# Performance work log

Hardware: AMD Instinct MI355X
Metric: run time of the kernel (lower is better)

## Reference

```python
import jax, jax.numpy as jnp
import numpy as np

N = 100000   # nodes
E = 1600000  # edges (avg degree 16)
D = 128      # feature dim (in_dim = out_dim = 128)


def setup_inputs() -> dict:
    key = jax.random.key(0)
    k0, k1, k2, k3, k4, k5 = jax.random.split(key, 6)
    x = jax.random.normal(k0, (N, D), dtype=jnp.float32)
    edge_index = jax.random.randint(k1, (2, E), 0, N, dtype=jnp.int32)
    # GCNConv linear weights (PyG stores lin.weight [out,in]; math is x @ W.T, here W:[in,out])
    s1 = 1.0 / np.sqrt(D)
    W1 = jax.random.uniform(k2, (D, D), jnp.float32, -s1, s1)
    b1 = jnp.zeros((D,), jnp.float32)
    W2 = jax.random.uniform(k3, (D, D), jnp.float32, -s1, s1)
    b2 = jnp.zeros((D,), jnp.float32)
    return {"x": x, "edge_index": edge_index, "W1": W1, "b1": b1, "W2": W2, "b2": b2}


def reference(x, edge_index, W1, b1, W2, b2):
    n = x.shape[0]
    idt = edge_index.dtype
    loop = jnp.arange(n, dtype=idt)
    src = jnp.concatenate([edge_index[0], loop])  # message sources
    dst = jnp.concatenate([edge_index[1], loop])  # aggregation targets
    # improved=True -> self-loop fill value 2.0; edge_weight=None -> ones
    w = jnp.concatenate([jnp.ones((edge_index.shape[1],), x.dtype),
                         jnp.full((n,), 2.0, x.dtype)])
    deg = jax.ops.segment_sum(w, dst, num_segments=n)
    dinv = jnp.where(deg > 0, jax.lax.rsqrt(deg), 0.0)
    norm = dinv[src] * w * dinv[dst]  # [E+N] symmetric GCN normalization

    def conv(h, W, b):
        h = h @ W  # [N, D] dense transform
        agg = jax.ops.segment_sum(norm[:, None] * h[src], dst, num_segments=n)
        return agg + b

    h = conv(x, W1, b1)        # conv1
    for _ in range(4):
        h = conv(h, W2, b2)
    return h
```

## Files before the change

### kernel.cpp

```cpp
#include <hip/hip_runtime.h>
#include <hip/hip_fp16.h>

#define D 128

typedef _Float16 half8 __attribute__((ext_vector_type(8)));
typedef float floatx4 __attribute__((ext_vector_type(4)));


__device__ inline void acc_h4(float& ax, float& ay, float& az, float& aw,
                              float w, uint2 raw) {
    __half2 h01 = *reinterpret_cast<const __half2*>(&raw.x);
    __half2 h23 = *reinterpret_cast<const __half2*>(&raw.y);
    ax = fmaf(w, __low2float(h01), ax);
    ay = fmaf(w, __high2float(h01), ay);
    az = fmaf(w, __low2float(h23), az);
    aw = fmaf(w, __high2float(h23), aw);
}


__global__ void k_zero(int* __restrict__ p, int n) {
    int i = blockIdx.x * 256 + threadIdx.x;
    if (i < n) p[i] = 0;
}

__global__ void k_count(const int* __restrict__ dst, int* __restrict__ cnt,
                        int* __restrict__ rank, int e) {
    int i = blockIdx.x * 256 + threadIdx.x;
    if (i < e) rank[i] = atomicAdd(&cnt[dst[i]], 1);
}

__global__ void k_f2h(const float* __restrict__ in, __half* __restrict__ out, int n8) {
    int i = blockIdx.x * 256 + threadIdx.x;
    if (i < n8) {
        const float4* p = (const float4*)in + (size_t)i * 2;
        float4 a = p[0], b = p[1];
        __half2 h0 = __float22half2_rn(make_float2(a.x, a.y));
        __half2 h1 = __float22half2_rn(make_float2(a.z, a.w));
        __half2 h2 = __float22half2_rn(make_float2(b.x, b.y));
        __half2 h3 = __float22half2_rn(make_float2(b.z, b.w));
        uint4 o;
        o.x = *(unsigned*)&h0; o.y = *(unsigned*)&h1;
        o.z = *(unsigned*)&h2; o.w = *(unsigned*)&h3;
        ((uint4*)out)[i] = o;
    }
}


__global__ __launch_bounds__(256) void k_scanA(const int* __restrict__ cnt,
                                               int* __restrict__ partials,
                                               float* __restrict__ dinv, int n) {
    __shared__ int s[256];
    int b = blockIdx.x, t = threadIdx.x;
    int i0 = b * 512 + t * 2;
    int v = 0;
    if (i0 < n) {
        int c0 = cnt[i0];
        v += c0;
        dinv[i0] = 1.0f / sqrtf((float)(c0 + 2));
    }
    if (i0 + 1 < n) {
        int c1 = cnt[i0 + 1];
        v += c1;
        dinv[i0 + 1] = 1.0f / sqrtf((float)(c1 + 2));
    }
    s[t] = v;
    __syncthreads();
    for (int off = 128; off > 0; off >>= 1) {
        if (t < off) s[t] += s[t + off];
        __syncthreads();
    }
    if (t == 0) partials[b] = s[0];
}

__global__ __launch_bounds__(512) void k_scanB(const int* __restrict__ partials,
                                               int* __restrict__ base,
                                               int* __restrict__ off_n, int nb) {
    __shared__ int s[512];
    int t = threadIdx.x;
    int v = (t < nb) ? partials[t] : 0;
    s[t] = v;
    __syncthreads();
    for (int off = 1; off < 512; off <<= 1) {
        int x = (t >= off) ? s[t - off] : 0;
        __syncthreads();
        s[t] += x;
        __syncthreads();
    }
    if (t < nb) base[t] = s[t] - v;
    if (t == nb - 1) off_n[0] = s[t];
}

__global__ __launch_bounds__(256) void k_scanC(const int* __restrict__ cnt,
                                               const int* __restrict__ base,
                                               int* __restrict__ offsets, int n) {
    __shared__ int s[256];
    int b = blockIdx.x, t = threadIdx.x;
    int i0 = b * 512 + t * 2;
    int v0 = (i0 < n) ? cnt[i0] : 0;
    int v1 = (i0 + 1 < n) ? cnt[i0 + 1] : 0;
    int sum = v0 + v1;
    s[t] = sum;
    __syncthreads();
    for (int off = 1; off < 256; off <<= 1) {
        int x = (t >= off) ? s[t - off] : 0;
        __syncthreads();
        s[t] += x;
        __syncthreads();
    }
    int excl = s[t] - sum + base[b];
    if (i0 < n) offsets[i0] = excl;
    if (i0 + 1 < n) offsets[i0 + 1] = excl + v0;
}

__global__ void k_fill(const int* __restrict__ src, const int* __restrict__ dst,
                       const int* __restrict__ rank, const int* __restrict__ offsets,
                       const float* __restrict__ dinv, int2* __restrict__ csr, int e) {
    int i = blockIdx.x * 256 + threadIdx.x;
    if (i < e) {
        int s = src[i];
        int d = dst[i];
        int pos = offsets[d] + rank[i];
        csr[pos] = make_int2(s, __float_as_int(dinv[s] * dinv[d]));
    }
}

__global__ __launch_bounds__(128) void k_wmm(const float* __restrict__ A,
                                             const float* __restrict__ B,
                                             float* __restrict__ Cm) {
    __shared__ float a[128];
    int r = blockIdx.x, d = threadIdx.x;
    a[d] = A[r * 128 + d];
    __syncthreads();
    float acc = 0.0f;
#pragma unroll 8
    for (int k = 0; k < 128; k++) acc += a[k] * B[k * 128 + d];
    Cm[r * 128 + d] = acc;
}

__global__ __launch_bounds__(128) void k_wmm_bias(const float* __restrict__ W1,
                                                  const float* __restrict__ W4,
                                                  const float* __restrict__ W2,
                                                  const float* __restrict__ b1,
                                                  const float* __restrict__ b2,
                                                  float* __restrict__ Wtot,
                                                  float* __restrict__ cmat) {
    __shared__ float s[128];
    int d = threadIdx.x;
    if (blockIdx.x < 128) {
        int r = blockIdx.x;
        s[d] = W1[r * 128 + d];
        __syncthreads();
        float acc = 0.0f;
#pragma unroll 8
        for (int k = 0; k < 128; k++) acc += s[k] * W4[k * 128 + d];
        Wtot[r * 128 + d] = acc;
        return;
    }
    float v = b2[d];
    cmat[d] = v;
    for (int j = 1; j <= 3; j++) {
        s[d] = v;
        __syncthreads();
        float acc = 0.0f;
#pragma unroll 8
        for (int k = 0; k < 128; k++) acc += s[k] * W2[k * 128 + d];
        v = acc;
        cmat[j * 128 + d] = v;
        __syncthreads();
    }
    s[d] = b1[d];
    __syncthreads();
    float acc = 0.0f;
#pragma unroll 8
    for (int k = 0; k < 128; k++) acc += s[k] * W4[k * 128 + d];
    cmat[4 * 128 + d] = acc;
}

__global__ __launch_bounds__(256) void k_wpack(const float* __restrict__ Wtot,
                                               __half* __restrict__ pack) {
    int tid = blockIdx.x * 256 + threadIdx.x;
    int l = tid & 63, t = (tid >> 6) & 7, s = tid >> 9;
    int col = t * 16 + (l & 15);
    int krow = s * 32 + 8 * (l >> 4);
#pragma unroll
    for (int j = 0; j < 8; j++) {
        float w = Wtot[(krow + j) * 128 + col];
        __half hh = __float2half(w);
        float rem = w - __half2float(hh);
        pack[(size_t)tid * 8 + j] = hh;
        pack[16384 + (size_t)tid * 8 + j] = __float2half(rem);
    }
}

__global__ __launch_bounds__(256) void k_matmul(const __half* __restrict__ Hh,
                                                const __half* __restrict__ Wpack,
                                                float* __restrict__ O,
                                                const float* __restrict__ ucol,
                                                const float* __restrict__ cmat,
                                                int nrows) {
    const int t = threadIdx.x;
    const int lane = t & 63, wave = t >> 6;
    const int rows0 = blockIdx.x * 64 + wave * 16;
    const int lrow = lane & 15, lk = lane >> 4;

    float uu[4][4];
#pragma unroll
    for (int r = 0; r < 4; r++) {
        int row = rows0 + lk * 4 + r;
        if (row >= nrows) row = nrows - 1;
#pragma unroll
        for (int tt = 0; tt < 4; tt++) uu[tt][r] = ucol[(size_t)tt * nrows + row];
    }

    floatx4 acc[8];
#pragma unroll
    for (int tl = 0; tl < 8; tl++) {
        int col = tl * 16 + lrow;
        float c0 = cmat[col];
        float c1 = cmat[128 + col], c2 = cmat[256 + col];
        float c3 = cmat[384 + col], c4 = cmat[512 + col];
#pragma unroll
        for (int r = 0; r < 4; r++)
            acc[tl][r] = c0 + uu[0][r] * c1 + uu[1][r] * c2
                            + uu[2][r] * c3 + uu[3][r] * c4;
    }

    int arow = rows0 + lrow;
    if (arow >= nrows) arow = nrows - 1;
    const __half* abase = Hh + (size_t)arow * 128 + lk * 8;

#pragma unroll
    for (int s = 0; s < 4; s++) {
        half8 a = *reinterpret_cast<const half8*>(abase + s * 32);
        const __half* wb = Wpack + (size_t)s * 4096 + (size_t)lane * 8;
#pragma unroll
        for (int tl = 0; tl < 8; tl++) {
            half8 bh = *reinterpret_cast<const half8*>(wb + (size_t)tl * 512);
            half8 bl = *reinterpret_cast<const half8*>(wb + (size_t)tl * 512 + 16384);
            acc[tl] = __builtin_amdgcn_mfma_f32_16x16x32_f16(a, bh, acc[tl], 0, 0, 0);
            acc[tl] = __builtin_amdgcn_mfma_f32_16x16x32_f16(a, bl, acc[tl], 0, 0, 0);
        }
    }

#pragma unroll
    for (int r = 0; r < 4; r++) {
        int row = rows0 + lk * 4 + r;
        if (row < nrows) {
            float* orow = O + (size_t)row * 128 + lrow;
#pragma unroll
            for (int tl = 0; tl < 8; tl++) orow[tl * 16] = acc[tl][r];
        }
    }
}

template <bool WITH_U, bool IN_F16, bool OUT_F16>
__global__ __launch_bounds__(256) void k_gather(const void* __restrict__ Tv,
                                                const int2* __restrict__ csr,
                                                const int* __restrict__ offsets,
                                                const float* __restrict__ dinv,
                                                void* __restrict__ Ov,
                                                const float* __restrict__ uin,
                                                float* __restrict__ uout, int n) {
    int node = blockIdx.x * 4 + (threadIdx.x >> 6);
    if (node >= n) return;
    int lane = threadIdx.x & 63;
    int hf = lane >> 5;
    int c = (lane & 31) << 2;
    const __half* Tch = (const __half*)Tv + c;
    const float*  Tcf = (const float*)Tv + c;

    float ax = 0.f, ay = 0.f, az = 0.f, aw = 0.f;
    float uacc = 0.f;
    if (hf == 0) {
        float di = dinv[node];
        float sw = 2.0f * di * di;
        if (IN_F16) {
            uint2 raw = *(const uint2*)(Tch + (size_t)node * D);
            acc_h4(ax, ay, az, aw, sw, raw);
        } else {
            float4 v = *(const float4*)(Tcf + (size_t)node * D);
            ax = sw * v.x; ay = sw * v.y; az = sw * v.z; aw = sw * v.w;
        }
        if (WITH_U) uacc = sw * (uin ? uin[node] : 1.0f);
    }

    int e = offsets[node];
    const int e1 = offsets[node + 1];

    for (; e + 8 <= e1; e += 8) {
        int2 p0 = csr[e + hf];
        int2 p1 = csr[e + 2 + hf];
        int2 p2 = csr[e + 4 + hf];
        int2 p3 = csr[e + 6 + hf];
        float w0 = __int_as_float(p0.y), w1 = __int_as_float(p1.y);
        float w2 = __int_as_float(p2.y), w3 = __int_as_float(p3.y);
        if (IN_F16) {
            uint2 r0 = *(const uint2*)(Tch + (size_t)p0.x * D);
            uint2 r1 = *(const uint2*)(Tch + (size_t)p1.x * D);
            uint2 r2 = *(const uint2*)(Tch + (size_t)p2.x * D);
            uint2 r3 = *(const uint2*)(Tch + (size_t)p3.x * D);
            if (WITH_U) {
                if (uin) {
                    uacc += w0 * uin[p0.x] + w1 * uin[p1.x]
                          + w2 * uin[p2.x] + w3 * uin[p3.x];
                } else {
                    uacc += w0 + w1 + w2 + w3;
                }
            }
            acc_h4(ax, ay, az, aw, w0, r0);
            acc_h4(ax, ay, az, aw, w1, r1);
            acc_h4(ax, ay, az, aw, w2, r2);
            acc_h4(ax, ay, az, aw, w3, r3);
        } else {
            float4 v0 = *(const float4*)(Tcf + (size_t)p0.x * D);
            float4 v1 = *(const float4*)(Tcf + (size_t)p1.x * D);
            float4 v2 = *(const float4*)(Tcf + (size_t)p2.x * D);
            float4 v3 = *(const float4*)(Tcf + (size_t)p3.x * D);
            if (WITH_U) {
                if (uin) {
                    uacc += w0 * uin[p0.x] + w1 * uin[p1.x]
                          + w2 * uin[p2.x] + w3 * uin[p3.x];
                } else {
                    uacc += w0 + w1 + w2 + w3;
                }
            }
            ax += w0 * v0.x; ay += w0 * v0.y; az += w0 * v0.z; aw += w0 * v0.w;
            ax += w1 * v1.x; ay += w1 * v1.y; az += w1 * v1.z; aw += w1 * v1.w;
            ax += w2 * v2.x; ay += w2 * v2.y; az += w2 * v2.z; aw += w2 * v2.w;
            ax += w3 * v3.x; ay += w3 * v3.y; az += w3 * v3.z; aw += w3 * v3.w;
        }
    }
    for (; e + 2 <= e1; e += 2) {
        int2 p0 = csr[e + hf];
        float w0 = __int_as_float(p0.y);
        if (WITH_U) uacc += w0 * (uin ? uin[p0.x] : 1.0f);
        if (IN_F16) {
            uint2 r0 = *(const uint2*)(Tch + (size_t)p0.x * D);
            acc_h4(ax, ay, az, aw, w0, r0);
        } else {
            float4 v0 = *(const float4*)(Tcf + (size_t)p0.x * D);
            ax += w0 * v0.x; ay += w0 * v0.y; az += w0 * v0.z; aw += w0 * v0.w;
        }
    }
    if (e < e1 && hf == 0) {
        int2 p0 = csr[e];
        float w0 = __int_as_float(p0.y);
        if (WITH_U) uacc += w0 * (uin ? uin[p0.x] : 1.0f);
        if (IN_F16) {
            uint2 r0 = *(const uint2*)(Tch + (size_t)p0.x * D);
            acc_h4(ax, ay, az, aw, w0, r0);
        } else {
            float4 v0 = *(const float4*)(Tcf + (size_t)p0.x * D);
            ax += w0 * v0.x; ay += w0 * v0.y; az += w0 * v0.z; aw += w0 * v0.w;
        }
    }

    ax += __shfl_xor(ax, 32, 64);
    ay += __shfl_xor(ay, 32, 64);
    az += __shfl_xor(az, 32, 64);
    aw += __shfl_xor(aw, 32, 64);
    if (WITH_U) uacc += __shfl_xor(uacc, 32, 64);

    if (hf == 0) {
        if (OUT_F16) {
            __half2 o01 = __float22half2_rn(make_float2(ax, ay));
            __half2 o23 = __float22half2_rn(make_float2(az, aw));
            float2 raw;
            *(__half2*)&raw.x = o01;
            *(__half2*)&raw.y = o23;
            *(float2*)((__half*)Ov + (size_t)node * D + c) = raw;
        } else {
            *(float4*)((float*)Ov + (size_t)node * D + c) =
                make_float4(ax, ay, az, aw);
        }
        if (WITH_U && lane == 0) uout[node] = uacc;
    }
}


extern "C" void kernel_launch(void* const* d_in, const int* in_sizes, int n_in,
                              void* d_out, int out_size, void* d_ws, size_t ws_size,
                              hipStream_t stream) {
    const float* x  = (const float*)d_in[0];
    const int*   ei = (const int*)d_in[1];
    const float* W1 = (const float*)d_in[2];
    const float* b1 = (const float*)d_in[3];
    const float* W2 = (const float*)d_in[4];
    const float* b2 = (const float*)d_in[5];
    const int N = in_sizes[0] / D;
    const int E = in_sizes[1] / 2;
    float* out = (float*)d_out;

    char* ws = (char*)d_ws;
    size_t woff = 0;
    auto alloc = [&](size_t bytes) -> void* {
        void* p = ws + woff;
        woff = (woff + bytes + 15) & ~(size_t)15;
        return p;
    };
    __half* T16a    = (__half*)alloc((size_t)N * D * sizeof(__half));
    __half* T16b    = (__half*)alloc((size_t)N * D * sizeof(__half));
    int*   cnt      = (int*)  alloc((size_t)N * sizeof(int));
    int*   offsets  = (int*)  alloc((size_t)(N + 1) * sizeof(int));
    int*   rank     = (int*)  alloc((size_t)E * sizeof(int));
    float* dinv     = (float*)alloc((size_t)N * sizeof(float));
    int2*  csr      = (int2*) alloc((size_t)E * sizeof(int2));
    int*   partials = (int*)  alloc(1024 * sizeof(int));
    int*   base     = (int*)  alloc(1024 * sizeof(int));
    float* ucol     = (float*)alloc((size_t)4 * N * sizeof(float));
    float* cmat     = (float*)alloc(5 * 128 * sizeof(float));
    float* Wsq      = (float*)alloc(128 * 128 * sizeof(float));
    float* W4      = (float*)alloc(128 * 128 * sizeof(float));
    float* Wtot     = (float*)alloc(128 * 128 * sizeof(float));
    __half* Wpack   = (__half*)alloc(32768 * sizeof(__half));
    size_t x16_bytes = (size_t)N * D * sizeof(__half);
    bool use_x16 = (woff + x16_bytes) <= ws_size;
    __half* X16 = use_x16 ? (__half*)alloc(x16_bytes) : nullptr;
    (void)n_in; (void)out_size;

    const int* e_src = ei;
    const int* e_dst = ei + E;
    const int NB = (N + 511) / 512;

    k_zero<<<(N + 255) / 256, 256, 0, stream>>>(cnt, N);
    k_count<<<(E + 255) / 256, 256, 0, stream>>>(e_dst, cnt, rank, E);
    k_scanA<<<NB, 256, 0, stream>>>(cnt, partials, dinv, N);
    k_scanB<<<1, 512, 0, stream>>>(partials, base, offsets + N, NB);
    k_scanC<<<NB, 256, 0, stream>>>(cnt, base, offsets, N);
    k_fill<<<(E + 255) / 256, 256, 0, stream>>>(e_src, e_dst, rank, offsets,
                                                dinv, csr, E);

    const int GG = (N + 3) / 4;
    if (use_x16) {
        int n8 = (N * D) / 8;
        k_f2h<<<(n8 + 255) / 256, 256, 0, stream>>>(x, X16, n8);
        k_gather<true, true, true><<<GG, 256, 0, stream>>>(
            X16, csr, offsets, dinv, T16a, nullptr, ucol, N);
    } else {
        k_gather<true, false, true><<<GG, 256, 0, stream>>>(
            x, csr, offsets, dinv, T16a, nullptr, ucol, N);
    }
    k_gather<true,  true, true><<<GG, 256, 0, stream>>>(
        T16a, csr, offsets, dinv, T16b, ucol,         ucol + N,     N);
    k_gather<true,  true, true><<<GG, 256, 0, stream>>>(
        T16b, csr, offsets, dinv, T16a, ucol + N,     ucol + 2 * N, N);
    k_gather<true,  true, true><<<GG, 256, 0, stream>>>(
        T16a, csr, offsets, dinv, T16b, ucol + 2 * N, ucol + 3 * N, N);
    k_gather<false, true, true><<<GG, 256, 0, stream>>>(
        T16b, csr, offsets, dinv, T16a, nullptr,      nullptr,      N);

    k_wmm<<<128, 128, 0, stream>>>(W2, W2, Wsq);
    k_wmm<<<128, 128, 0, stream>>>(Wsq, Wsq, W4);
    k_wmm_bias<<<129, 128, 0, stream>>>(W1, W4, W2, b1, b2, Wtot, cmat);
    k_wpack<<<8, 256, 0, stream>>>(Wtot, Wpack);

    k_matmul<<<(N + 63) / 64, 256, 0, stream>>>(T16a, Wpack, out, ucol, cmat, N);
}
```

Baseline: 658.2 us.

## Store fp16 features in 8 column-sliced planes for cache-local gathers

Features are stored as 8 slices of 16 columns each (slice-major, then node), and the gather kernel launches 8 blocks per node group. Each block processes one slice, so the active working set per slice is N×32 bytes and can fit in L2/LLC. Each wave handles one node, with 8 edge groups of 8 lanes, each lane covering 2 columns, and a shuffle reduction at the end. The conversion and matmul kernels are updated to read this layout. The trade-off is 8× more reads of CSR, offsets and dinv, plus smaller 4-byte scattered loads.

```diff
diff --git a/kernel.cpp b/kernel.cpp
--- a/kernel.cpp
+++ b/kernel.cpp
@@ -5,17 +5,6 @@
 
 typedef _Float16 half8 __attribute__((ext_vector_type(8)));
 typedef float floatx4 __attribute__((ext_vector_type(4)));
-
-
-__device__ inline void acc_h4(float& ax, float& ay, float& az, float& aw,
-                              float w, uint2 raw) {
-    __half2 h01 = *reinterpret_cast<const __half2*>(&raw.x);
-    __half2 h23 = *reinterpret_cast<const __half2*>(&raw.y);
-    ax = fmaf(w, __low2float(h01), ax);
-    ay = fmaf(w, __high2float(h01), ay);
-    az = fmaf(w, __low2float(h23), az);
-    aw = fmaf(w, __high2float(h23), aw);
-}
 
 
 __global__ void k_zero(int* __restrict__ p, int n) {
@@ -29,20 +18,28 @@
     if (i < e) rank[i] = atomicAdd(&cnt[dst[i]], 1);
 }
 
-__global__ void k_f2h(const float* __restrict__ in, __half* __restrict__ out, int n8) {
+__global__ void k_f2h_s(const float* __restrict__ in, __half* __restrict__ out,
+                        int n) {
     int i = blockIdx.x * 256 + threadIdx.x;
-    if (i < n8) {
-        const float4* p = (const float4*)in + (size_t)i * 2;
-        float4 a = p[0], b = p[1];
-        __half2 h0 = __float22half2_rn(make_float2(a.x, a.y));
-        __half2 h1 = __float22half2_rn(make_float2(a.z, a.w));
-        __half2 h2 = __float22half2_rn(make_float2(b.x, b.y));
-        __half2 h3 = __float22half2_rn(make_float2(b.z, b.w));
-        uint4 o;
-        o.x = *(unsigned*)&h0; o.y = *(unsigned*)&h1;
-        o.z = *(unsigned*)&h2; o.w = *(unsigned*)&h3;
-        ((uint4*)out)[i] = o;
-    }
+    if (i >= n * 8) return;
+    int node = i >> 3, slice = i & 7;
+    const float4* p = (const float4*)(in + (size_t)node * D + slice * 16);
+    float4 a = p[0], b = p[1], c = p[2], d = p[3];
+    __half2 h0 = __float22half2_rn(make_float2(a.x, a.y));
+    __half2 h1 = __float22half2_rn(make_float2(a.z, a.w));
+    __half2 h2 = __float22half2_rn(make_float2(b.x, b.y));
+    __half2 h3 = __float22half2_rn(make_float2(b.z, b.w));
+    __half2 h4 = __float22half2_rn(make_float2(c.x, c.y));
+    __half2 h5 = __float22half2_rn(make_float2(c.z, c.w));
+    __half2 h6 = __float22half2_rn(make_float2(d.x, d.y));
+    __half2 h7 = __float22half2_rn(make_float2(d.z, d.w));
+    uint4* o = (uint4*)(out + ((size_t)slice * n + node) * 16);
+    uint4 o0, o1;
+    o0.x = *(unsigned*)&h0; o0.y = *(unsigned*)&h1;
+    o0.z = *(unsigned*)&h2; o0.w = *(unsigned*)&h3;
+    o1.x = *(unsigned*)&h4; o1.y = *(unsigned*)&h5;
+    o1.z = *(unsigned*)&h6; o1.w = *(unsigned*)&h7;
+    o[0] = o0; o[1] = o1;
 }
 
 
@@ -227,11 +224,12 @@
 
     int arow = rows0 + lrow;
     if (arow >= nrows) arow = nrows - 1;
-    const __half* abase = Hh + (size_t)arow * 128 + lk * 8;
 
 #pragma unroll
     for (int s = 0; s < 4; s++) {
-        half8 a = *reinterpret_cast<const half8*>(abase + s * 32);
+        int slice = 2 * s + (lk >> 1);
+        const __half* ap = Hh + ((size_t)slice * nrows + arow) * 16 + (lk & 1) * 8;
+        half8 a = *reinterpret_cast<const half8*>(ap);
         const __half* wb = Wpack + (size_t)s * 4096 + (size_t)lane * 8;
 #pragma unroll
         for (int tl = 0; tl < 8; tl++) {
@@ -253,127 +251,95 @@
     }
 }
 
-template <bool WITH_U, bool IN_F16, bool OUT_F16>
-__global__ __launch_bounds__(256) void k_gather(const void* __restrict__ Tv,
-                                                const int2* __restrict__ csr,
-                                                const int* __restrict__ offsets,
-                                                const float* __restrict__ dinv,
-                                                void* __restrict__ Ov,
-                                                const float* __restrict__ uin,
-                                                float* __restrict__ uout, int n) {
-    int node = blockIdx.x * 4 + (threadIdx.x >> 6);
+template <bool WITH_U, bool IN_ROWMAJOR_F32>
+__global__ __launch_bounds__(256) void k_gather_s(const void* __restrict__ Tv,
+                                                  const int2* __restrict__ csr,
+                                                  const int* __restrict__ offsets,
+                                                  const float* __restrict__ dinv,
+                                                  __half* __restrict__ Ov,
+                                                  const float* __restrict__ uin,
+                                                  float* __restrict__ uout, int n) {
+    const int slice = blockIdx.x & 7;
+    const int node = (blockIdx.x >> 3) * 4 + (threadIdx.x >> 6);
     if (node >= n) return;
-    int lane = threadIdx.x & 63;
-    int hf = lane >> 5;
-    int c = (lane & 31) << 2;
-    const __half* Tch = (const __half*)Tv + c;
-    const float*  Tcf = (const float*)Tv + c;
-
-    float ax = 0.f, ay = 0.f, az = 0.f, aw = 0.f;
-    float uacc = 0.f;
-    if (hf == 0) {
-        float di = dinv[node];
-        float sw = 2.0f * di * di;
-        if (IN_F16) {
-            uint2 raw = *(const uint2*)(Tch + (size_t)node * D);
-            acc_h4(ax, ay, az, aw, sw, raw);
+    const int lane = threadIdx.x & 63;
+    const int g = lane >> 3;
+    const int p = lane & 7;
+    const bool do_u = WITH_U && (slice == 0);
+
+    const __half* Ts = (const __half*)Tv + (((size_t)slice * n) << 4) + (p << 1);
+    const float*  Xs = (const float*)Tv + (size_t)(slice * 16 + p * 2);
+
+    float dn = dinv[node];
+    float sw = 2.0f * dn * dn;
+    float a0 = 0.f, a1 = 0.f, uacc = 0.f;
+
+    if (g == 0) {
+        if (IN_ROWMAJOR_F32) {
+            float2 v = *(const float2*)(Xs + (size_t)node * D);
+            a0 = sw * v.x; a1 = sw * v.y;
         } else {
-            float4 v = *(const float4*)(Tcf + (size_t)node * D);
-            ax = sw * v.x; ay = sw * v.y; az = sw * v.z; aw = sw * v.w;
-        }
-        if (WITH_U) uacc = sw * (uin ? uin[node] : 1.0f);
+            unsigned raw = *(const unsigned*)(Ts + ((size_t)node << 4));
+            __half2 h = *reinterpret_cast<const __half2*>(&raw);
+            a0 = sw * __low2float(h); a1 = sw * __high2float(h);
+        }
+        if (do_u && p == 0) uacc = sw * (uin ? uin[node] : 1.0f);
     }
 
     int e = offsets[node];
     const int e1 = offsets[node + 1];
 
-    for (; e + 8 <= e1; e += 8) {
-        int2 p0 = csr[e + hf];
-        int2 p1 = csr[e + 2 + hf];
-        int2 p2 = csr[e + 4 + hf];
-        int2 p3 = csr[e + 6 + hf];
-        float w0 = __int_as_float(p0.y), w1 = __int_as_float(p1.y);
-        float w2 = __int_as_float(p2.y), w3 = __int_as_float(p3.y);
-        if (IN_F16) {
-            uint2 r0 = *(const uint2*)(Tch + (size_t)p0.x * D);
-            uint2 r1 = *(const uint2*)(Tch + (size_t)p1.x * D);
-            uint2 r2 = *(const uint2*)(Tch + (size_t)p2.x * D);
-            uint2 r3 = *(const uint2*)(Tch + (size_t)p3.x * D);
-            if (WITH_U) {
-                if (uin) {
-                    uacc += w0 * uin[p0.x] + w1 * uin[p1.x]
-                          + w2 * uin[p2.x] + w3 * uin[p3.x];
-                } else {
-                    uacc += w0 + w1 + w2 + w3;
-                }
-            }
-            acc_h4(ax, ay, az, aw, w0, r0);
-            acc_h4(ax, ay, az, aw, w1, r1);
-            acc_h4(ax, ay, az, aw, w2, r2);
-            acc_h4(ax, ay, az, aw, w3, r3);
+    for (; e + 16 <= e1; e += 16) {
+        int2 pa = csr[e + g];
+        int2 pb = csr[e + 8 + g];
+        float wa = __int_as_float(pa.y), wb = __int_as_float(pb.y);
+        if (IN_ROWMAJOR_F32) {
+            float2 va = *(const float2*)(Xs + (size_t)pa.x * D);
+            float2 vb = *(const float2*)(Xs + (size_t)pb.x * D);
+            a0 = fmaf(wa, va.x, a0); a1 = fmaf(wa, va.y, a1);
+            a0 = fmaf(wb, vb.x, a0); a1 = fmaf(wb, vb.y, a1);
         } else {
-            float4 v0 = *(const float4*)(Tcf + (size_t)p0.x * D);
-            float4 v1 = *(const float4*)(Tcf + (size_t)p1.x * D);
-            float4 v2 = *(const float4*)(Tcf + (size_t)p2.x * D);
-            float4 v3 = *(const float4*)(Tcf + (size_t)p3.x * D);
-            if (WITH_U) {
-                if (uin) {
-                    uacc += w0 * uin[p0.x] + w1 * uin[p1.x]
-                          + w2 * uin[p2.x] + w3 * uin[p3.x];
-                } else {
-                    uacc += w0 + w1 + w2 + w3;
-                }
-            }
-            ax += w0 * v0.x; ay += w0 * v0.y; az += w0 * v0.z; aw += w0 * v0.w;
-            ax += w1 * v1.x; ay += w1 * v1.y; az += w1 * v1.z; aw += w1 * v1.w;
-            ax += w2 * v2.x; ay += w2 * v2.y; az += w2 * v2.z; aw += w2 * v2.w;
-            ax += w3 * v3.x; ay += w3 * v3.y; az += w3 * v3.z; aw += w3 * v3.w;
-        }
-    }
-    for (; e + 2 <= e1; e += 2) {
-        int2 p0 = csr[e + hf];
-        float w0 = __int_as_float(p0.y);
-        if (WITH_U) uacc += w0 * (uin ? uin[p0.x] : 1.0f);
-        if (IN_F16) {
-            uint2 r0 = *(const uint2*)(Tch + (size_t)p0.x * D);
-            acc_h4(ax, ay, az, aw, w0, r0);
+            unsigned ra = *(const unsigned*)(Ts + ((size_t)pa.x << 4));
+            unsigned rb = *(const unsigned*)(Ts + ((size_t)pb.x << 4));
+            __half2 ha = *reinterpret_cast<const __half2*>(&ra);
+            __half2 hb = *reinterpret_cast<const __half2*>(&rb);
+            a0 = fmaf(wa, __low2float(ha), a0); a1 = fmaf(wa, __high2float(ha), a1);
+            a0 = fmaf(wb, __low2float(hb), a0); a1 = fmaf(wb, __high2float(hb), a1);
+        }
+        if (do_u && p == 0) {
+            uacc = fmaf(wa, uin ? uin[pa.x] : 1.0f, uacc);
+            uacc = fmaf(wb, uin ? uin[pb.x] : 1.0f, uacc);
+        }
+    }
+    for (; e < e1; e += 8) {
+        int idx = e + g;
+        bool ok = idx < e1;
+        int2 pa = csr[ok ? idx : e];
+        float wa = ok ? __int_as_float(pa.y) : 0.0f;
+        if (IN_ROWMAJOR_F32) {
+            float2 va = *(const float2*)(Xs + (size_t)pa.x * D);
+            a0 = fmaf(wa, va.x, a0); a1 = fmaf(wa, va.y, a1);
         } else {
-            float4 v0 = *(const float4*)(Tcf + (size_t)p0.x * D);
-            ax += w0 * v0.x; ay += w0 * v0.y; az += w0 * v0.z; aw += w0 * v0.w;
-        }
-    }
-    if (e < e1 && hf == 0) {
-        int2 p0 = csr[e];
-        float w0 = __int_as_float(p0.y);
-        if (WITH_U) uacc += w0 * (uin ? uin[p0.x] : 1.0f);
-        if (IN_F16) {
-            uint2 r0 = *(const uint2*)(Tch + (size_t)p0.x * D);
-            acc_h4(ax, ay, az, aw, w0, r0);
-        } else {
-            float4 v0 = *(const float4*)(Tcf + (size_t)p0.x * D);
-            ax += w0 * v0.x; ay += w0 * v0.y; az += w0 * v0.z; aw += w0 * v0.w;
-        }
-    }
-
-    ax += __shfl_xor(ax, 32, 64);
-    ay += __shfl_xor(ay, 32, 64);
-    az += __shfl_xor(az, 32, 64);
-    aw += __shfl_xor(aw, 32, 64);
-    if (WITH_U) uacc += __shfl_xor(uacc, 32, 64);
-
-    if (hf == 0) {
-        if (OUT_F16) {
-            __half2 o01 = __float22half2_rn(make_float2(ax, ay));
-            __half2 o23 = __float22half2_rn(make_float2(az, aw));
-            float2 raw;
-            *(__half2*)&raw.x = o01;
-            *(__half2*)&raw.y = o23;
-            *(float2*)((__half*)Ov + (size_t)node * D + c) = raw;
-        } else {
-            *(float4*)((float*)Ov + (size_t)node * D + c) =
-                make_float4(ax, ay, az, aw);
-        }
-        if (WITH_U && lane == 0) uout[node] = uacc;
+            unsigned ra = *(const unsigned*)(Ts + ((size_t)pa.x << 4));
+            __half2 ha = *reinterpret_cast<const __half2*>(&ra);
+            a0 = fmaf(wa, __low2float(ha), a0); a1 = fmaf(wa, __high2float(ha), a1);
+        }
+        if (do_u && p == 0) uacc = fmaf(wa, uin ? uin[pa.x] : 1.0f, uacc);
+    }
+
+    a0 += __shfl_xor(a0, 8, 64);  a1 += __shfl_xor(a1, 8, 64);
+    a0 += __shfl_xor(a0, 16, 64); a1 += __shfl_xor(a1, 16, 64);
+    a0 += __shfl_xor(a0, 32, 64); a1 += __shfl_xor(a1, 32, 64);
+    if (do_u) {
+        uacc += __shfl_xor(uacc, 8, 64);
+        uacc += __shfl_xor(uacc, 16, 64);
+        uacc += __shfl_xor(uacc, 32, 64);
+    }
+
+    if (g == 0) {
+        __half2 o = __float22half2_rn(make_float2(a0, a1));
+        *(__half2*)(Ov + (((size_t)slice * n + node) << 4) + (p << 1)) = o;
+        if (do_u && lane == 0) uout[node] = uacc;
     }
 }
 
@@ -410,7 +376,7 @@
     float* ucol     = (float*)alloc((size_t)4 * N * sizeof(float));
     float* cmat     = (float*)alloc(5 * 128 * sizeof(float));
     float* Wsq      = (float*)alloc(128 * 128 * sizeof(float));
-    float* W4      = (float*)alloc(128 * 128 * sizeof(float));
+    float* W4       = (float*)alloc(128 * 128 * sizeof(float));
     float* Wtot     = (float*)alloc(128 * 128 * sizeof(float));
     __half* Wpack   = (__half*)alloc(32768 * sizeof(__half));
     size_t x16_bytes = (size_t)N * D * sizeof(__half);
@@ -430,23 +396,22 @@
     k_fill<<<(E + 255) / 256, 256, 0, stream>>>(e_src, e_dst, rank, offsets,
                                                 dinv, csr, E);
 
-    const int GG = (N + 3) / 4;
+    const int GG = ((N + 3) / 4) * 8;
     if (use_x16) {
-        int n8 = (N * D) / 8;
-        k_f2h<<<(n8 + 255) / 256, 256, 0, stream>>>(x, X16, n8);
-        k_gather<true, true, true><<<GG, 256, 0, stream>>>(
+        k_f2h_s<<<(N * 8 + 255) / 256, 256, 0, stream>>>(x, X16, N);
+        k_gather_s<true, false><<<GG, 256, 0, stream>>>(
             X16, csr, offsets, dinv, T16a, nullptr, ucol, N);
     } else {
-        k_gather<true, false, true><<<GG, 256, 0, stream>>>(
+        k_gather_s<true, true><<<GG, 256, 0, stream>>>(
             x, csr, offsets, dinv, T16a, nullptr, ucol, N);
     }
-    k_gather<true,  true, true><<<GG, 256, 0, stream>>>(
+    k_gather_s<true,  false><<<GG, 256, 0, stream>>>(
         T16a, csr, offsets, dinv, T16b, ucol,         ucol + N,     N);
-    k_gather<true,  true, true><<<GG, 256, 0, stream>>>(
+    k_gather_s<true,  false><<<GG, 256, 0, stream>>>(
         T16b, csr, offsets, dinv, T16a, ucol + N,     ucol + 2 * N, N);
-    k_gather<true,  true, true><<<GG, 256, 0, stream>>>(
+    k_gather_s<true,  false><<<GG, 256, 0, stream>>>(
         T16a, csr, offsets, dinv, T16b, ucol + 2 * N, ucol + 3 * N, N);
-    k_gather<false, true, true><<<GG, 256, 0, stream>>>(
+    k_gather_s<false, false><<<GG, 256, 0, stream>>>(
         T16b, csr, offsets, dinv, T16a, nullptr,      nullptr,      N);
 
     k_wmm<<<128, 128, 0, stream>>>(W2, W2, Wsq);
```

New measurement: 1.612 ms. 2.45x slower.
